# Kernel tuning notes

Hardware: AMD Instinct MI355X
Metric: run time of the kernel (lower is better)

Reference implementation:

```python
import jax, jax.numpy as jnp
import numpy as np

N_NODES = 50000
N_EDGES = 500000
D_FEAT = 128


def setup_inputs() -> dict:
    key = jax.random.key(0)
    k1, k2 = jax.random.split(key)
    x = jax.random.normal(k1, (N_NODES, D_FEAT), dtype=jnp.float32)
    edge_index = jax.random.randint(k2, (2, N_EDGES), 0, N_NODES, dtype=jnp.int64)
    return {"x": x, "edge_index": edge_index}


def reference(x, edge_index):
    # flow='source_to_target': row = edge_index[0] (source j), col = edge_index[1] (target i)
    row, col = edge_index[0], edge_index[1]
    # message(x_j) = x_j ; aggregate = scatter-add at target indices ; update = identity
    messages = jnp.take(x, row, axis=0)            # [E, D] gather
    out = jax.ops.segment_sum(messages, col, num_segments=x.shape[0])  # [N, D]
    return out
```

## Files before the change

### kernel.cpp

```cpp
#include <hip/hip_runtime.h>
#include <hip/hip_bf16.h>


#define D_FEAT 128
#define MAXDEG 32

typedef unsigned short u16;
typedef unsigned int u32;

__device__ __forceinline__ u16 f2bf(float f) {
    __hip_bfloat16 h = __float2bfloat16(f);
    union { __hip_bfloat16 h; u16 u; } c; c.h = h;
    return c.u;
}
__device__ __forceinline__ float bf2f(u16 u) {
    return __uint_as_float(((u32)u) << 16);
}

__global__ __launch_bounds__(256) void prep_kernel(const float* __restrict__ x,
                                                   int* __restrict__ cnt, int zc4,
                                                   u16* __restrict__ xb, int nf4) {
    const int t = blockIdx.x * blockDim.x + threadIdx.x;
    if (t < zc4) {
        reinterpret_cast<int4*>(cnt)[t] = make_int4(0, 0, 0, 0);
    } else {
        const int i = t - zc4;
        if (i < nf4) {
            const float4 v = reinterpret_cast<const float4*>(x)[i];
            ushort4 o;
            o.x = f2bf(v.x); o.y = f2bf(v.y); o.z = f2bf(v.z); o.w = f2bf(v.w);
            reinterpret_cast<ushort4*>(xb)[i] = o;
        }
    }
}

__global__ __launch_bounds__(256) void fillb_kernel(const int* __restrict__ row,
                                                    const int* __restrict__ col,
                                                    int* __restrict__ cnt,
                                                    u16* __restrict__ srclist,
                                                    int* __restrict__ ovf,
                                                    int* __restrict__ ovfcnt,
                                                    int E, int ovfcap, int aligned) {
    const int t = blockIdx.x * blockDim.x + threadIdx.x;
    const int e0 = t * 4;
    if (e0 >= E) return;

    int d[4], s[4], p[4], ne;
    if (aligned && e0 + 4 <= E) {
        const int4 dv = *reinterpret_cast<const int4*>(col + e0);
        const int4 sv = *reinterpret_cast<const int4*>(row + e0);
        d[0] = dv.x; d[1] = dv.y; d[2] = dv.z; d[3] = dv.w;
        s[0] = sv.x; s[1] = sv.y; s[2] = sv.z; s[3] = sv.w;
        ne = 4;
    } else {
        ne = E - e0; if (ne > 4) ne = 4;
        for (int k = 0; k < ne; ++k) { d[k] = col[e0 + k]; s[k] = row[e0 + k]; }
    }
    #pragma unroll
    for (int k = 0; k < 4; ++k)
        if (k < ne) p[k] = atomicAdd(&cnt[d[k]], 1);
    #pragma unroll
    for (int k = 0; k < 4; ++k) {
        if (k < ne) {
            if (p[k] < MAXDEG) {
                srclist[(size_t)d[k] * MAXDEG + p[k]] = (u16)s[k];
            } else {
                int o = atomicAdd(ovfcnt, 1);
                if (o < ovfcap) { ovf[2 * o] = d[k]; ovf[2 * o + 1] = s[k]; }
            }
        }
    }
}

__global__ __launch_bounds__(256) void gatherb_kernel(const u16* __restrict__ xb,
                                                      const int* __restrict__ cnt,
                                                      const u16* __restrict__ srclist,
                                                      const int* __restrict__ ovf,
                                                      const int* __restrict__ ovfcnt,
                                                      float* __restrict__ out,
                                                      int N, int ovfcap) {
    const int wid  = (blockIdx.x * blockDim.x + threadIdx.x) >> 6;
    const int lane = threadIdx.x & 63;
    if (wid >= N) return;
    const int slot = lane >> 5;
    const int c    = lane & 31;
    const int rawdeg = cnt[wid];
    const int deg = rawdeg > MAXDEG ? MAXDEG : rawdeg;
    const u16* bucket = srclist + (size_t)wid * MAXDEG;
    const int bval = bucket[c];

    float4 acc = {0.f, 0.f, 0.f, 0.f};
    int j = 0;
    for (; j + 4 <= deg; j += 4) {
        const int i0 = __shfl(bval, j + slot, 64);
        const int i1 = __shfl(bval, j + 2 + slot, 64);
        const ushort4 v0 = *reinterpret_cast<const ushort4*>(xb + (size_t)i0 * D_FEAT + c * 4);
        const ushort4 v1 = *reinterpret_cast<const ushort4*>(xb + (size_t)i1 * D_FEAT + c * 4);
        acc.x += bf2f(v0.x) + bf2f(v1.x);
        acc.y += bf2f(v0.y) + bf2f(v1.y);
        acc.z += bf2f(v0.z) + bf2f(v1.z);
        acc.w += bf2f(v0.w) + bf2f(v1.w);
    }
    if (j + 2 <= deg) {
        const int i0 = __shfl(bval, j + slot, 64);
        const ushort4 v0 = *reinterpret_cast<const ushort4*>(xb + (size_t)i0 * D_FEAT + c * 4);
        acc.x += bf2f(v0.x); acc.y += bf2f(v0.y); acc.z += bf2f(v0.z); acc.w += bf2f(v0.w);
        j += 2;
    }
    if (j < deg && slot == 0) {
        const int i0 = __shfl(bval, j, 64);
        const ushort4 v0 = *reinterpret_cast<const ushort4*>(xb + (size_t)i0 * D_FEAT + c * 4);
        acc.x += bf2f(v0.x); acc.y += bf2f(v0.y); acc.z += bf2f(v0.z); acc.w += bf2f(v0.w);
    }

    if (rawdeg > MAXDEG) {
        int novf = *ovfcnt;
        if (novf > ovfcap) novf = ovfcap;
        for (int k = 0; k < novf; ++k) {
            if (ovf[2 * k] == wid && slot == 0) {
                const int s = ovf[2 * k + 1];
                const ushort4 v = *reinterpret_cast<const ushort4*>(xb + (size_t)s * D_FEAT + c * 4);
                acc.x += bf2f(v.x); acc.y += bf2f(v.y); acc.z += bf2f(v.z); acc.w += bf2f(v.w);
            }
        }
    }

    acc.x += __shfl_xor(acc.x, 32, 64);
    acc.y += __shfl_xor(acc.y, 32, 64);
    acc.z += __shfl_xor(acc.z, 32, 64);
    acc.w += __shfl_xor(acc.w, 32, 64);
    if (slot == 0)
        *reinterpret_cast<float4*>(out + (size_t)wid * D_FEAT + c * 4) = acc;
}

__global__ void mp_scatter_kernel(const float* __restrict__ x,
                                  const int* __restrict__ row,
                                  const int* __restrict__ col,
                                  float* __restrict__ out, int n_edges) {
    const int t = blockIdx.x * blockDim.x + threadIdx.x;
    const int e = t >> 5;
    const int c = t & 31;
    if (e >= n_edges) return;
    const float4 v = *reinterpret_cast<const float4*>(
        x + (size_t)row[e] * D_FEAT + (size_t)c * 4);
    float* o = out + (size_t)col[e] * D_FEAT + (size_t)c * 4;
    atomicAdd(o + 0, v.x);
    atomicAdd(o + 1, v.y);
    atomicAdd(o + 2, v.z);
    atomicAdd(o + 3, v.w);
}

extern "C" void kernel_launch(void* const* d_in, const int* in_sizes, int n_in,
                              void* d_out, int out_size, void* d_ws, size_t ws_size,
                              hipStream_t stream) {
    const float* x   = (const float*)d_in[0];
    const int*   ei  = (const int*)d_in[1];
    float*       out = (float*)d_out;

    const int E = in_sizes[1] / 2;
    const int N = out_size / D_FEAT;
    const int* row = ei;
    const int* col = ei + E;

    const size_t cnt_ints  = ((size_t)N + 1 + 63) & ~(size_t)63;
    const size_t xb_off    = (cnt_ints * 4 + 255) & ~(size_t)255;
    const size_t xb_bytes  = (size_t)N * D_FEAT * 2;
    const size_t src_off   = (xb_off + xb_bytes + 255) & ~(size_t)255;
    const size_t src_bytes = (size_t)N * MAXDEG * 2;
    const size_t ovf_off   = (src_off + src_bytes + 255) & ~(size_t)255;
    const size_t needed    = ovf_off + 2ull * (size_t)E * 4;

    if (ws_size < needed || N > 65535) {
        hipMemsetAsync(d_out, 0, (size_t)out_size * sizeof(float), stream);
        const int total = E * 32;
        mp_scatter_kernel<<<(total + 255) / 256, 256, 0, stream>>>(x, row, col, out, E);
        return;
    }

    char* wsb     = (char*)d_ws;
    int*  cnt     = (int*)wsb;
    int*  ovfcnt  = cnt + N;
    u16*  xb      = (u16*)(wsb + xb_off);
    u16*  srclist = (u16*)(wsb + src_off);
    int*  ovf     = (int*)(wsb + ovf_off);

    const int zc4 = (int)(cnt_ints / 4);
    const int nf4 = N * D_FEAT / 4;
    const int prep_threads = zc4 + nf4;
    prep_kernel<<<(prep_threads + 255) / 256, 256, 0, stream>>>(x, cnt, zc4, xb, nf4);

    const int aligned = ((E & 3) == 0) ? 1 : 0;
    const int fill_threads = (E + 3) / 4;
    fillb_kernel<<<(fill_threads + 255) / 256, 256, 0, stream>>>(row, col, cnt, srclist,
                                                                 ovf, ovfcnt, E, E, aligned);

    const int total = N * 64;
    gatherb_kernel<<<(total + 255) / 256, 256, 0, stream>>>(xb, cnt, srclist,
                                                            ovf, ovfcnt, out, N, E);
}
```

Measured before the change: 126.1 us.

## Fuse bucket fill with bf16 conversion and widen gather loads to 16 bytes

The count array is now zeroed with a memset, and the edge bucketing and fp32-to-bf16 conversion run as separate block ranges of one fused launch, so the two independent stages can overlap. The gather kernel splits each wavefront into four 16-lane quarters. Each lane loads 8 bf16 values (16 bytes) per row, so four neighbour rows are processed in parallel, followed by a two-step cross-quarter shuffle reduction. This adds register pressure (8 accumulators) and a memset launch in exchange for fewer kernel boundaries and wider memory transactions.

```diff
diff --git a/kernel.cpp b/kernel.cpp
--- a/kernel.cpp
+++ b/kernel.cpp
@@ -9,22 +9,61 @@
 typedef unsigned int u32;
 
 __device__ __forceinline__ u16 f2bf(float f) {
-    __hip_bfloat16 h = __float2bfloat16(f);
-    union { __hip_bfloat16 h; u16 u; } c; c.h = h;
+    union { __hip_bfloat16 h; u16 u; } c;
+    c.h = __float2bfloat16(f);
     return c.u;
 }
-__device__ __forceinline__ float bf2f(u16 u) {
-    return __uint_as_float(((u32)u) << 16);
-}
-
-__global__ __launch_bounds__(256) void prep_kernel(const float* __restrict__ x,
-                                                   int* __restrict__ cnt, int zc4,
-                                                   u16* __restrict__ xb, int nf4) {
-    const int t = blockIdx.x * blockDim.x + threadIdx.x;
-    if (t < zc4) {
-        reinterpret_cast<int4*>(cnt)[t] = make_int4(0, 0, 0, 0);
+__device__ __forceinline__ float bflo(u32 u) { return __uint_as_float(u << 16); }
+__device__ __forceinline__ float bfhi(u32 u) { return __uint_as_float(u & 0xffff0000u); }
+
+__device__ __forceinline__ void addrow(float acc[8], const uint4& v) {
+    acc[0] += bflo(v.x); acc[1] += bfhi(v.x);
+    acc[2] += bflo(v.y); acc[3] += bfhi(v.y);
+    acc[4] += bflo(v.z); acc[5] += bfhi(v.z);
+    acc[6] += bflo(v.w); acc[7] += bfhi(v.w);
+}
+
+__global__ __launch_bounds__(256) void fused_kernel(const float* __restrict__ x,
+                                                    u16* __restrict__ xb, int nf4,
+                                                    const int* __restrict__ row,
+                                                    const int* __restrict__ col,
+                                                    int* __restrict__ cnt,
+                                                    u16* __restrict__ srclist,
+                                                    int* __restrict__ ovf,
+                                                    int* __restrict__ ovfcnt,
+                                                    int E, int ovfcap,
+                                                    int fill_blocks, int aligned) {
+    if ((int)blockIdx.x < fill_blocks) {
+        const int t = blockIdx.x * 256 + threadIdx.x;
+        const int e0 = t * 4;
+        if (e0 >= E) return;
+        int d[4], s[4], p[4], ne;
+        if (aligned && e0 + 4 <= E) {
+            const int4 dv = *reinterpret_cast<const int4*>(col + e0);
+            const int4 sv = *reinterpret_cast<const int4*>(row + e0);
+            d[0] = dv.x; d[1] = dv.y; d[2] = dv.z; d[3] = dv.w;
+            s[0] = sv.x; s[1] = sv.y; s[2] = sv.z; s[3] = sv.w;
+            ne = 4;
+        } else {
+            ne = E - e0; if (ne > 4) ne = 4;
+            for (int k = 0; k < ne; ++k) { d[k] = col[e0 + k]; s[k] = row[e0 + k]; }
+        }
+        #pragma unroll
+        for (int k = 0; k < 4; ++k)
+            if (k < ne) p[k] = atomicAdd(&cnt[d[k]], 1);
+        #pragma unroll
+        for (int k = 0; k < 4; ++k) {
+            if (k < ne) {
+                if (p[k] < MAXDEG) {
+                    srclist[(size_t)d[k] * MAXDEG + p[k]] = (u16)s[k];
+                } else {
+                    int o = atomicAdd(ovfcnt, 1);
+                    if (o < ovfcap) { ovf[2 * o] = d[k]; ovf[2 * o + 1] = s[k]; }
+                }
+            }
+        }
     } else {
-        const int i = t - zc4;
+        const int i = ((int)blockIdx.x - fill_blocks) * 256 + threadIdx.x;
         if (i < nf4) {
             const float4 v = reinterpret_cast<const float4*>(x)[i];
             ushort4 o;
@@ -34,45 +73,7 @@
     }
 }
 
-__global__ __launch_bounds__(256) void fillb_kernel(const int* __restrict__ row,
-                                                    const int* __restrict__ col,
-                                                    int* __restrict__ cnt,
-                                                    u16* __restrict__ srclist,
-                                                    int* __restrict__ ovf,
-                                                    int* __restrict__ ovfcnt,
-                                                    int E, int ovfcap, int aligned) {
-    const int t = blockIdx.x * blockDim.x + threadIdx.x;
-    const int e0 = t * 4;
-    if (e0 >= E) return;
-
-    int d[4], s[4], p[4], ne;
-    if (aligned && e0 + 4 <= E) {
-        const int4 dv = *reinterpret_cast<const int4*>(col + e0);
-        const int4 sv = *reinterpret_cast<const int4*>(row + e0);
-        d[0] = dv.x; d[1] = dv.y; d[2] = dv.z; d[3] = dv.w;
-        s[0] = sv.x; s[1] = sv.y; s[2] = sv.z; s[3] = sv.w;
-        ne = 4;
-    } else {
-        ne = E - e0; if (ne > 4) ne = 4;
-        for (int k = 0; k < ne; ++k) { d[k] = col[e0 + k]; s[k] = row[e0 + k]; }
-    }
-    #pragma unroll
-    for (int k = 0; k < 4; ++k)
-        if (k < ne) p[k] = atomicAdd(&cnt[d[k]], 1);
-    #pragma unroll
-    for (int k = 0; k < 4; ++k) {
-        if (k < ne) {
-            if (p[k] < MAXDEG) {
-                srclist[(size_t)d[k] * MAXDEG + p[k]] = (u16)s[k];
-            } else {
-                int o = atomicAdd(ovfcnt, 1);
-                if (o < ovfcap) { ovf[2 * o] = d[k]; ovf[2 * o + 1] = s[k]; }
-            }
-        }
-    }
-}
-
-__global__ __launch_bounds__(256) void gatherb_kernel(const u16* __restrict__ xb,
+__global__ __launch_bounds__(256) void gatherq_kernel(const u16* __restrict__ xb,
                                                       const int* __restrict__ cnt,
                                                       const u16* __restrict__ srclist,
                                                       const int* __restrict__ ovf,
@@ -82,55 +83,61 @@
     const int wid  = (blockIdx.x * blockDim.x + threadIdx.x) >> 6;
     const int lane = threadIdx.x & 63;
     if (wid >= N) return;
-    const int slot = lane >> 5;
-    const int c    = lane & 31;
+    const int q = lane >> 4;
+    const int c = lane & 15;
     const int rawdeg = cnt[wid];
     const int deg = rawdeg > MAXDEG ? MAXDEG : rawdeg;
     const u16* bucket = srclist + (size_t)wid * MAXDEG;
-    const int bval = bucket[c];
-
-    float4 acc = {0.f, 0.f, 0.f, 0.f};
+    const int bval = (int)bucket[lane & 31];
+
+    float acc[8] = {0.f, 0.f, 0.f, 0.f, 0.f, 0.f, 0.f, 0.f};
+
     int j = 0;
-    for (; j + 4 <= deg; j += 4) {
-        const int i0 = __shfl(bval, j + slot, 64);
-        const int i1 = __shfl(bval, j + 2 + slot, 64);
-        const ushort4 v0 = *reinterpret_cast<const ushort4*>(xb + (size_t)i0 * D_FEAT + c * 4);
-        const ushort4 v1 = *reinterpret_cast<const ushort4*>(xb + (size_t)i1 * D_FEAT + c * 4);
-        acc.x += bf2f(v0.x) + bf2f(v1.x);
-        acc.y += bf2f(v0.y) + bf2f(v1.y);
-        acc.z += bf2f(v0.z) + bf2f(v1.z);
-        acc.w += bf2f(v0.w) + bf2f(v1.w);
-    }
-    if (j + 2 <= deg) {
-        const int i0 = __shfl(bval, j + slot, 64);
-        const ushort4 v0 = *reinterpret_cast<const ushort4*>(xb + (size_t)i0 * D_FEAT + c * 4);
-        acc.x += bf2f(v0.x); acc.y += bf2f(v0.y); acc.z += bf2f(v0.z); acc.w += bf2f(v0.w);
-        j += 2;
-    }
-    if (j < deg && slot == 0) {
-        const int i0 = __shfl(bval, j, 64);
-        const ushort4 v0 = *reinterpret_cast<const ushort4*>(xb + (size_t)i0 * D_FEAT + c * 4);
-        acc.x += bf2f(v0.x); acc.y += bf2f(v0.y); acc.z += bf2f(v0.z); acc.w += bf2f(v0.w);
+    for (; j + 8 <= deg; j += 8) {
+        const int i0 = __shfl(bval, j + q, 64);
+        const int i1 = __shfl(bval, j + 4 + q, 64);
+        const uint4 w0 = *reinterpret_cast<const uint4*>(xb + (size_t)i0 * D_FEAT + c * 8);
+        const uint4 w1 = *reinterpret_cast<const uint4*>(xb + (size_t)i1 * D_FEAT + c * 8);
+        addrow(acc, w0);
+        addrow(acc, w1);
+    }
+    if (j + 4 <= deg) {
+        const int i0 = __shfl(bval, j + q, 64);
+        const uint4 w0 = *reinterpret_cast<const uint4*>(xb + (size_t)i0 * D_FEAT + c * 8);
+        addrow(acc, w0);
+        j += 4;
+    }
+    {
+        const int r = deg - j;
+        const int i0 = __shfl(bval, j + q, 64);
+        if (q < r) {
+            const uint4 w0 = *reinterpret_cast<const uint4*>(xb + (size_t)i0 * D_FEAT + c * 8);
+            addrow(acc, w0);
+        }
     }
 
     if (rawdeg > MAXDEG) {
         int novf = *ovfcnt;
         if (novf > ovfcap) novf = ovfcap;
         for (int k = 0; k < novf; ++k) {
-            if (ovf[2 * k] == wid && slot == 0) {
+            if (ovf[2 * k] == wid && q == 0) {
                 const int s = ovf[2 * k + 1];
-                const ushort4 v = *reinterpret_cast<const ushort4*>(xb + (size_t)s * D_FEAT + c * 4);
-                acc.x += bf2f(v.x); acc.y += bf2f(v.y); acc.z += bf2f(v.z); acc.w += bf2f(v.w);
+                const uint4 w = *reinterpret_cast<const uint4*>(xb + (size_t)s * D_FEAT + c * 8);
+                addrow(acc, w);
             }
         }
     }
 
-    acc.x += __shfl_xor(acc.x, 32, 64);
-    acc.y += __shfl_xor(acc.y, 32, 64);
-    acc.z += __shfl_xor(acc.z, 32, 64);
-    acc.w += __shfl_xor(acc.w, 32, 64);
-    if (slot == 0)
-        *reinterpret_cast<float4*>(out + (size_t)wid * D_FEAT + c * 4) = acc;
+    #pragma unroll
+    for (int k = 0; k < 8; ++k) {
+        acc[k] += __shfl_xor(acc[k], 16, 64);
+        acc[k] += __shfl_xor(acc[k], 32, 64);
+    }
+    if (q == 0) {
+        float* o = out + (size_t)wid * D_FEAT + c * 8;
+        *reinterpret_cast<float4*>(o)     = make_float4(acc[0], acc[1], acc[2], acc[3]);
+        *reinterpret_cast<float4*>(o + 4) = make_float4(acc[4], acc[5], acc[6], acc[7]);
+    }
 }
 
 __global__ void mp_scatter_kernel(const float* __restrict__ x,
@@ -162,8 +169,8 @@
     const int* row = ei;
     const int* col = ei + E;
 
-    const size_t cnt_ints  = ((size_t)N + 1 + 63) & ~(size_t)63;
-    const size_t xb_off    = (cnt_ints * 4 + 255) & ~(size_t)255;
+    const size_t cnt_bytes = ((size_t)N + 1) * 4;
+    const size_t xb_off    = (cnt_bytes + 255) & ~(size_t)255;
     const size_t xb_bytes  = (size_t)N * D_FEAT * 2;
     const size_t src_off   = (xb_off + xb_bytes + 255) & ~(size_t)255;
     const size_t src_bytes = (size_t)N * MAXDEG * 2;
@@ -171,7 +178,7 @@
     const size_t needed    = ovf_off + 2ull * (size_t)E * 4;
 
     if (ws_size < needed || N > 65535) {
-        hipMemsetAsync(d_out, 0, (size_t)out_size * sizeof(float), stream);
+        (void)hipMemsetAsync(d_out, 0, (size_t)out_size * sizeof(float), stream);
         const int total = E * 32;
         mp_scatter_kernel<<<(total + 255) / 256, 256, 0, stream>>>(x, row, col, out, E);
         return;
@@ -184,17 +191,17 @@
     u16*  srclist = (u16*)(wsb + src_off);
     int*  ovf     = (int*)(wsb + ovf_off);
 
-    const int zc4 = (int)(cnt_ints / 4);
-    const int nf4 = N * D_FEAT / 4;
-    const int prep_threads = zc4 + nf4;
-    prep_kernel<<<(prep_threads + 255) / 256, 256, 0, stream>>>(x, cnt, zc4, xb, nf4);
-
-    const int aligned = ((E & 3) == 0) ? 1 : 0;
+    (void)hipMemsetAsync(cnt, 0, cnt_bytes, stream);
+
     const int fill_threads = (E + 3) / 4;
-    fillb_kernel<<<(fill_threads + 255) / 256, 256, 0, stream>>>(row, col, cnt, srclist,
-                                                                 ovf, ovfcnt, E, E, aligned);
+    const int fill_blocks  = (fill_threads + 255) / 256;
+    const int nf4          = N * D_FEAT / 4;
+    const int conv_blocks  = (nf4 + 255) / 256;
+    const int aligned      = ((E & 3) == 0) ? 1 : 0;
+    fused_kernel<<<fill_blocks + conv_blocks, 256, 0, stream>>>(
+        x, xb, nf4, row, col, cnt, srclist, ovf, ovfcnt, E, E, fill_blocks, aligned);
 
     const int total = N * 64;
-    gatherb_kernel<<<(total + 255) / 256, 256, 0, stream>>>(xb, cnt, srclist,
+    gatherq_kernel<<<(total + 255) / 256, 256, 0, stream>>>(xb, cnt, srclist,
                                                             ovf, ovfcnt, out, N, E);
 }
```

Result: no change. 125.9 us (median of 2 runs) (-0.2%).
